# Performance work log

Measured on AMD Instinct MI355X. Metric: run time of the kernel, lower is better.

The kernel has to match this reference:

```python
import jax, jax.numpy as jnp
import numpy as np

H, W = 32, 32
DIM = 768
NUM_BLOCKS = 4
BLOCK = DIM // NUM_BLOCKS
SCALE = 0.02


def setup_inputs() -> dict:
    key = jax.random.key(0)
    k0, k1, k2, k3, k4 = jax.random.split(key, 5)
    B, N, C = 64, H * W, DIM
    x = jax.random.normal(k0, (B, N, C), dtype=jnp.float32)
    w1 = SCALE * jax.random.normal(k1, (2, NUM_BLOCKS, BLOCK, BLOCK), dtype=jnp.float32)
    b1 = SCALE * jax.random.normal(k2, (2, NUM_BLOCKS, BLOCK), dtype=jnp.float32)
    w2 = SCALE * jax.random.normal(k3, (2, NUM_BLOCKS, BLOCK, BLOCK), dtype=jnp.float32)
    b2 = SCALE * jax.random.normal(k4, (2, NUM_BLOCKS, BLOCK), dtype=jnp.float32)
    return {"x": x, "w1": w1, "b1": b1, "w2": w2, "b2": b2}


def _mul(inp, weights):
    # inp: [B, H, Wf, blocks, d], weights: [blocks, d, k]
    return jnp.einsum('...bd,bdk->...bk', inp, weights)


def reference(x, w1, b1, w2, b2):
    B, N, C = x.shape
    xg = x.reshape(B, H, W, C)
    xf = jnp.fft.rfft2(xg, axes=(1, 2), norm='ortho')  # [B, H, W//2+1, C] complex64
    xf = xf.reshape(B, xf.shape[1], xf.shape[2], NUM_BLOCKS, BLOCK)
    xr, xi = xf.real, xf.imag
    # layer 1: complex block-diagonal linear + ReLU
    r1 = jax.nn.relu(_mul(xr, w1[0]) - _mul(xi, w1[1]) + b1[0])
    i1 = jax.nn.relu(_mul(xr, w1[1]) + _mul(xi, w1[0]) + b1[1])
    # layer 2 (faithful to original: imag uses the already-updated real part)
    r2 = _mul(r1, w2[0]) - _mul(i1, w2[1]) + b2[0]
    i2 = _mul(r2, w2[1]) + _mul(i1, w2[0]) + b2[1]
    xc = (r2 + 1j * i2).reshape(B, r2.shape[1], r2.shape[2], C)
    out = jnp.fft.irfft2(xc, s=(H, W), axes=(1, 2), norm='ortho')
    return out.reshape(B, N, C) + jnp.zeros_like(x)  # bias is zeros (self.bias is None)
```

## Files before the change

kernel.cpp:

```cpp
#include <hip/hip_runtime.h>
#include <cstddef>
#include <cstdint>


typedef __attribute__((ext_vector_type(8))) short bf16x8;
typedef __attribute__((ext_vector_type(4))) float f32x4;

namespace {

constexpr int BATCH = 64;
constexpr int WF    = 17;
constexpr int CC    = 768;
constexpr int BLK   = 192;

constexpr size_t W_ELEMS  = 16u * 36864u;
constexpr size_t TW_ELEMS = 8u * 1024u;
constexpr size_t PW_ELEMS = W_ELEMS + TW_ELEMS;

constexpr int PLANE_U = 48 * 512;

constexpr float C32[32] = {
   1.0000000000f,  0.9807852804f,  0.9238795325f,  0.8314696123f,
   0.7071067812f,  0.5555702330f,  0.3826834324f,  0.1950903220f,
   0.0000000000f, -0.1950903220f, -0.3826834324f, -0.5555702330f,
  -0.7071067812f, -0.8314696123f, -0.9238795325f, -0.9807852804f,
  -1.0000000000f, -0.9807852804f, -0.9238795325f, -0.8314696123f,
  -0.7071067812f, -0.5555702330f, -0.3826834324f, -0.1950903220f,
   0.0000000000f,  0.1950903220f,  0.3826834324f,  0.5555702330f,
   0.7071067812f,  0.8314696123f,  0.9238795325f,  0.9807852804f
};
constexpr float S32[32] = {
   0.0000000000f,  0.1950903220f,  0.3826834324f,  0.5555702330f,
   0.7071067812f,  0.8314696123f,  0.9238795325f,  0.9807852804f,
   1.0000000000f,  0.9807852804f,  0.9238795325f,  0.8314696123f,
   0.7071067812f,  0.5555702330f,  0.3826834324f,  0.1950903220f,
   0.0000000000f, -0.1950903220f, -0.3826834324f, -0.5555702330f,
  -0.7071067812f, -0.8314696123f, -0.9238795325f, -0.9807852804f,
  -1.0000000000f, -0.9807852804f, -0.9238795325f, -0.8314696123f,
  -0.7071067812f, -0.5555702330f, -0.3826834324f, -0.1950903220f
};

}

__device__ __forceinline__ ushort f2bf(float f) {
    union { float f; unsigned u; } v; v.f = f;
    const unsigned r = (v.u + 0x7FFFu + ((v.u >> 16) & 1u)) >> 16;
    return (ushort)r;
}
__device__ __forceinline__ uint pk(float lo, float hi) {
    return (uint)f2bf(lo) | ((uint)f2bf(hi) << 16);
}
__device__ __forceinline__ bf16x8 neg8(bf16x8 a) {
    union { bf16x8 v; uint4 u; } t; t.v = a;
    t.u.x ^= 0x80008000u; t.u.y ^= 0x80008000u;
    t.u.z ^= 0x80008000u; t.u.w ^= 0x80008000u;
    return t.v;
}

__global__ __launch_bounds__(256) void k_pack(const float* __restrict__ w1,
                                              const float* __restrict__ w2,
                                              ushort* __restrict__ pw) {
    const unsigned idx = blockIdx.x * 256u + threadIdx.x;
    if (idx < W_ELEMS) {
        const unsigned mi = idx / 36864u;
        const unsigned r  = idx % 36864u;
        const unsigned kk = r / 6144u;
        const unsigned r2 = r % 6144u;
        const unsigned nf = r2 / 512u;
        const unsigned r3 = r2 % 512u;
        const unsigned lane = r3 / 8u;
        const unsigned i  = r3 % 8u;
        const unsigned d   = kk * 32u + (lane >> 4) * 8u + i;
        const unsigned col = nf * 16u + (lane & 15u);
        const unsigned mat = mi >> 2, blk = mi & 3u;
        const float* src;
        if      (mat == 0u) src = w1 + (size_t)(0 * 4 + blk) * BLK * BLK;
        else if (mat == 1u) src = w1 + (size_t)(1 * 4 + blk) * BLK * BLK;
        else if (mat == 2u) src = w2 + (size_t)(0 * 4 + blk) * BLK * BLK;
        else                src = w2 + (size_t)(1 * 4 + blk) * BLK * BLK;
        pw[idx] = f2bf(src[(size_t)d * BLK + col]);
    } else if (idx < PW_ELEMS) {
        const unsigned t = idx - (unsigned)W_ELEMS;
        const unsigned mat = t >> 10;
        const unsigned rr  = t & 1023u;
        const unsigned mf  = rr >> 9;
        const unsigned q   = rr & 511u;
        const unsigned lane = q >> 3, i = q & 7u;
        const unsigned row = mf * 16u + (lane & 15u);
        const unsigned col = (lane >> 4) * 8u + i;
        const unsigned ang = (row * col) & 31u;
        float v;
        if      (mat == 0u) v = C32[ang] * 0.03125f;
        else if (mat == 1u) v = S32[ang] * 0.03125f;
        else if (mat == 2u) v = -S32[ang] * 0.03125f;
        else if (mat == 3u) v = C32[ang];
        else if (mat == 4u) v = S32[ang];
        else if (mat == 5u) v = -S32[ang];
        else if (mat == 6u) {
            if      (col == 0u)  v = 0.03125f;
            else if (col < 16u)  v = 2.f * C32[ang] * 0.03125f;
            else if (col == 16u) v = C32[(16u * row) & 31u] * 0.03125f;
            else                 v = 0.f;
        } else {
            v = (col >= 1u && col <= 15u) ? (-2.f * S32[ang] * 0.03125f) : 0.f;
        }
        pw[idx] = f2bf(v);
    }
}

__global__ __launch_bounds__(256) void k_rfft_w(const float* __restrict__ x,
                                                ushort* __restrict__ spec,
                                                const ushort* __restrict__ pw) {
    __shared__ uint xb[16 * 384];

    const int bid = blockIdx.x;
    const int cq = bid & 3;
    const int hp = (bid >> 2) & 15;
    const int b  = bid >> 6;
    const int tid = threadIdx.x;
    const int wv = tid >> 6, l = tid & 63, lc = l & 15, lg = l >> 4;

#pragma unroll
    for (int it = 0; it < 6; ++it) {
        const int flat = it * 256 + tid;
        const int h  = flat / 768;
        const int rm = flat % 768;
        const int wp = rm / 48;
        const int c4 = rm % 48;
        const float* p = x + ((size_t)(b * 1024 + (hp * 2 + h) * 32 + wp * 2) * CC)
                           + cq * 192 + c4 * 4;
        const float4 a  = *(const float4*)p;
        const float4 bb = *(const float4*)(p + CC);
        uint4 u;
        u.x = pk(a.x, bb.x); u.y = pk(a.y, bb.y);
        u.z = pk(a.z, bb.z); u.w = pk(a.w, bb.w);
        const int col = (h * 192 + c4 * 4) ^ (((wp >> 2) & 3) << 3);
        *(uint4*)&xb[wp * 384 + col] = u;
    }
    __syncthreads();

    const ushort* TW = pw + W_ELEMS;
    bf16x8 ac[2], as[2];
#pragma unroll
    for (int m = 0; m < 2; ++m) {
        ac[m] = *(const bf16x8*)(TW + ((size_t)(3 * 2 + m) * 64 + l) * 8);
        as[m] = *(const bf16x8*)(TW + ((size_t)(5 * 2 + m) * 64 + l) * 8);
    }

    f32x4 aR[2][6] = {}, aI[2][6] = {};
#pragma unroll
    for (int j = 0; j < 6; ++j) {
        const int nf = (j < 3) ? (wv * 3 + j) : (12 + wv * 3 + (j - 3));
        union { bf16x8 v; uint d[4]; } u;
#pragma unroll
        for (int t = 0; t < 4; ++t) {
            const int wp = lg * 4 + t;
            u.d[t] = xb[wp * 384 + ((nf * 16 + lc) ^ (lg << 3))];
        }
#pragma unroll
        for (int m = 0; m < 2; ++m) {
            aR[m][j] = __builtin_amdgcn_mfma_f32_16x16x32_bf16(ac[m], u.v, aR[m][j], 0, 0, 0);
            aI[m][j] = __builtin_amdgcn_mfma_f32_16x16x32_bf16(as[m], u.v, aI[m][j], 0, 0, 0);
        }
    }

    uint* spec32 = (uint*)spec;
    const int swz = (hp & 7) << 1;
#pragma unroll
    for (int m = 0; m < 2; ++m)
#pragma unroll
        for (int j = 0; j < 3; ++j)
#pragma unroll
            for (int r = 0; r < 4; ++r) {
                if (m == 1 && (lg != 0 || r != 0)) continue;
                const int kw = m * 16 + lg * 4 + r;
                const int csub = cq * 12 + wv * 3 + j;
                const size_t pos = ((size_t)(b * WF + kw) * 2) * 12288
                                 + csub * 256 + hp * 16 + (lc ^ swz);
                spec32[pos]         = pk(aR[m][j][r], aR[m][j + 3][r]);
                spec32[pos + 12288] = pk(aI[m][j][r], aI[m][j + 3][r]);
            }
}

__global__ __launch_bounds__(256, 4) void k_fft_mix(
        ushort* __restrict__ spec,
        const ushort* __restrict__ pw,
        const float* __restrict__ b1, const float* __restrict__ b2) {

    __shared__ ushort lds[3][6336];

    const int bid = blockIdx.x;
    const int blk = bid / (BATCH * WF);
    const int rem = bid % (BATCH * WF);
    const int b   = rem / WF;
    const int kw  = rem % WF;
    const int tid = threadIdx.x;
    const int wv = tid >> 6, l = tid & 63, lc = l & 15, lg = l >> 4;

    const size_t gR = ((size_t)(b * WF + kw) * 2) * PLANE_U + blk * 6144;
    const size_t gI = gR + PLANE_U;

#pragma unroll
    for (int j = 0; j < 3; ++j) {
        const int q = tid + 256 * j;
        const int dst = (q >> 6) * 528 + (q & 63) * 8;
        *(uint4*)&lds[0][dst] = *(const uint4*)(spec + gR + q * 8);
        *(uint4*)&lds[1][dst] = *(const uint4*)(spec + gI + q * 8);
    }
    __syncthreads();

    const ushort* TW = pw + W_ELEMS;
    const int col0 = wv * 48;

    {
        bf16x8 xr[3], xi[3];
#pragma unroll
        for (int n = 0; n < 3; ++n) {
            const int csub = wv * 3 + n;
            union { bf16x8 v; uint d[4]; } ur, ui;
#pragma unroll
            for (int t = 0; t < 4; ++t) {
                const int hp = lg * 4 + t;
                const int pos = csub * 528 + hp * 32 + ((lc ^ ((hp & 7) << 1)) << 1);
                ur.d[t] = *(const uint*)&lds[0][pos];
                ui.d[t] = *(const uint*)&lds[1][pos];
            }
            xr[n] = ur.v; xi[n] = ui.v;
        }
        bf16x8 cf[2], sf[2], sfn[2];
#pragma unroll
        for (int m = 0; m < 2; ++m) {
            cf[m]  = *(const bf16x8*)(TW + ((size_t)(0 * 2 + m) * 64 + l) * 8);
            sf[m]  = *(const bf16x8*)(TW + ((size_t)(1 * 2 + m) * 64 + l) * 8);
            sfn[m] = *(const bf16x8*)(TW + ((size_t)(2 * 2 + m) * 64 + l) * 8);
        }
        f32x4 yr[2][3] = {}, yi[2][3] = {};
#pragma unroll
        for (int m = 0; m < 2; ++m)
#pragma unroll
            for (int n = 0; n < 3; ++n) {
                yr[m][n] = __builtin_amdgcn_mfma_f32_16x16x32_bf16(cf[m],  xr[n], yr[m][n], 0, 0, 0);
                yr[m][n] = __builtin_amdgcn_mfma_f32_16x16x32_bf16(sf[m],  xi[n], yr[m][n], 0, 0, 0);
                yi[m][n] = __builtin_amdgcn_mfma_f32_16x16x32_bf16(cf[m],  xi[n], yi[m][n], 0, 0, 0);
                yi[m][n] = __builtin_amdgcn_mfma_f32_16x16x32_bf16(sfn[m], xr[n], yi[m][n], 0, 0, 0);
            }
#pragma unroll
        for (int m = 0; m < 2; ++m)
#pragma unroll
            for (int n = 0; n < 3; ++n)
#pragma unroll
                for (int rp = 0; rp < 2; ++rp) {
                    const uint ur = pk(yr[m][n][2 * rp], yr[m][n][2 * rp + 1]);
                    const uint ui = pk(yi[m][n][2 * rp], yi[m][n][2 * rp + 1]);
                    const int p0 = (wv * 3 + n) * 528 + (m * 16 + lg * 4 + 2 * rp) * 16 + lc;
                    lds[0][p0] = (ushort)ur; lds[0][p0 + 16] = (ushort)(ur >> 16);
                    lds[1][p0] = (ushort)ui; lds[1][p0 + 16] = (ushort)(ui >> 16);
                }
    }
    __syncthreads();

    const ushort* pW1r = pw + (size_t)(0 * 4 + blk) * 36864;
    const ushort* pW1i = pw + (size_t)(1 * 4 + blk) * 36864;
    const ushort* pW2r = pw + (size_t)(2 * 4 + blk) * 36864;
    const ushort* pW2i = pw + (size_t)(3 * 4 + blk) * 36864;

    {
        f32x4 aR[2][3], aI[2][3];
#pragma unroll
        for (int n = 0; n < 3; ++n) {
            const float br = b1[(size_t)(0 * 4 + blk) * BLK + col0 + n * 16 + lc];
            const float bi = b1[(size_t)(1 * 4 + blk) * BLK + col0 + n * 16 + lc];
#pragma unroll
            for (int m = 0; m < 2; ++m) {
                aR[m][n] = (f32x4){br, br, br, br};
                aI[m][n] = (f32x4){bi, bi, bi, bi};
            }
        }
#pragma unroll
        for (int kk = 0; kk < 6; ++kk) {
            const int csubA = 2 * kk + (lg >> 1);
            const int apos  = csubA * 528 + lc * 16 + (lg & 1) * 8;
            bf16x8 ar[2], ai[2], ain[2];
#pragma unroll
            for (int m = 0; m < 2; ++m) {
                ar[m]  = *(const bf16x8*)&lds[0][apos + m * 256];
                ai[m]  = *(const bf16x8*)&lds[1][apos + m * 256];
                ain[m] = neg8(ai[m]);
            }
            bf16x8 wr[3], wi[3];
#pragma unroll
            for (int n = 0; n < 3; ++n) {
                const size_t off = ((size_t)(kk * 12 + wv * 3 + n) * 64 + l) * 8;
                wr[n] = *(const bf16x8*)(pW1r + off);
                wi[n] = *(const bf16x8*)(pW1i + off);
            }
#pragma unroll
            for (int m = 0; m < 2; ++m)
#pragma unroll
                for (int n = 0; n < 3; ++n) {
                    aR[m][n] = __builtin_amdgcn_mfma_f32_16x16x32_bf16(ar[m],  wr[n], aR[m][n], 0, 0, 0);
                    aR[m][n] = __builtin_amdgcn_mfma_f32_16x16x32_bf16(ain[m], wi[n], aR[m][n], 0, 0, 0);
                    aI[m][n] = __builtin_amdgcn_mfma_f32_16x16x32_bf16(ar[m],  wi[n], aI[m][n], 0, 0, 0);
                    aI[m][n] = __builtin_amdgcn_mfma_f32_16x16x32_bf16(ai[m],  wr[n], aI[m][n], 0, 0, 0);
                }
        }
        __syncthreads();
#pragma unroll
        for (int m = 0; m < 2; ++m)
#pragma unroll
            for (int n = 0; n < 3; ++n)
#pragma unroll
                for (int rp = 0; rp < 2; ++rp) {
                    const uint ur = pk(fmaxf(aR[m][n][2 * rp], 0.f), fmaxf(aR[m][n][2 * rp + 1], 0.f));
                    const uint ui = pk(fmaxf(aI[m][n][2 * rp], 0.f), fmaxf(aI[m][n][2 * rp + 1], 0.f));
                    const int p0 = (wv * 3 + n) * 528 + (m * 16 + lg * 4 + 2 * rp) * 16 + lc;
                    lds[0][p0] = (ushort)ur; lds[0][p0 + 16] = (ushort)(ur >> 16);
                    lds[1][p0] = (ushort)ui; lds[1][p0 + 16] = (ushort)(ui >> 16);
                }
    }
    __syncthreads();

    {
        f32x4 cR[2][3];
#pragma unroll
        for (int n = 0; n < 3; ++n) {
            const float br = b2[(size_t)(0 * 4 + blk) * BLK + col0 + n * 16 + lc];
#pragma unroll
            for (int m = 0; m < 2; ++m) cR[m][n] = (f32x4){br, br, br, br};
        }
#pragma unroll
        for (int kk = 0; kk < 6; ++kk) {
            const int csubA = 2 * kk + (lg >> 1);
            const int apos  = csubA * 528 + lc * 16 + (lg & 1) * 8;
            bf16x8 ar[2], ain[2];
#pragma unroll
            for (int m = 0; m < 2; ++m) {
                ar[m]  = *(const bf16x8*)&lds[0][apos + m * 256];
                ain[m] = neg8(*(const bf16x8*)&lds[1][apos + m * 256]);
            }
            bf16x8 wr[3], wi[3];
#pragma unroll
            for (int n = 0; n < 3; ++n) {
                const size_t off = ((size_t)(kk * 12 + wv * 3 + n) * 64 + l) * 8;
                wr[n] = *(const bf16x8*)(pW2r + off);
                wi[n] = *(const bf16x8*)(pW2i + off);
            }
#pragma unroll
            for (int m = 0; m < 2; ++m)
#pragma unroll
                for (int n = 0; n < 3; ++n) {
                    cR[m][n] = __builtin_amdgcn_mfma_f32_16x16x32_bf16(ar[m],  wr[n], cR[m][n], 0, 0, 0);
                    cR[m][n] = __builtin_amdgcn_mfma_f32_16x16x32_bf16(ain[m], wi[n], cR[m][n], 0, 0, 0);
                }
        }
        __syncthreads();
#pragma unroll
        for (int m = 0; m < 2; ++m)
#pragma unroll
            for (int n = 0; n < 3; ++n) {
                const int csub = wv * 3 + n;
#pragma unroll
                for (int rp = 0; rp < 2; ++rp) {
                    const uint p = pk(cR[m][n][2 * rp], cR[m][n][2 * rp + 1]);
                    const int kh0 = m * 16 + lg * 4 + 2 * rp;
                    lds[0][csub * 528 + kh0 * 16 + lc]       = (ushort)p;
                    lds[0][csub * 528 + (kh0 + 1) * 16 + lc] = (ushort)(p >> 16);
                    const int hp = kh0 >> 1;
                    const int post = csub * 528 + hp * 32 + ((lc ^ ((hp & 7) << 1)) << 1);
                    *(uint*)&lds[2][post] = p;
                }
            }
    }
    __syncthreads();

    {
        f32x4 cI[2][3];
#pragma unroll
        for (int n = 0; n < 3; ++n) {
            const float bi = b2[(size_t)(1 * 4 + blk) * BLK + col0 + n * 16 + lc];
#pragma unroll
            for (int m = 0; m < 2; ++m) cI[m][n] = (f32x4){bi, bi, bi, bi};
        }
#pragma unroll
        for (int kk = 0; kk < 6; ++kk) {
            const int csubA = 2 * kk + (lg >> 1);
            const int apos  = csubA * 528 + lc * 16 + (lg & 1) * 8;
            bf16x8 a2[2], i1[2];
#pragma unroll
            for (int m = 0; m < 2; ++m) {
                a2[m] = *(const bf16x8*)&lds[0][apos + m * 256];
                i1[m] = *(const bf16x8*)&lds[1][apos + m * 256];
            }
            bf16x8 wi[3], wr[3];
#pragma unroll
            for (int n = 0; n < 3; ++n) {
                const size_t off = ((size_t)(kk * 12 + wv * 3 + n) * 64 + l) * 8;
                wi[n] = *(const bf16x8*)(pW2i + off);
                wr[n] = *(const bf16x8*)(pW2r + off);
            }
#pragma unroll
            for (int m = 0; m < 2; ++m)
#pragma unroll
                for (int n = 0; n < 3; ++n) {
                    cI[m][n] = __builtin_amdgcn_mfma_f32_16x16x32_bf16(a2[m], wi[n], cI[m][n], 0, 0, 0);
                    cI[m][n] = __builtin_amdgcn_mfma_f32_16x16x32_bf16(i1[m], wr[n], cI[m][n], 0, 0, 0);
                }
        }
        __syncthreads();
#pragma unroll
        for (int m = 0; m < 2; ++m)
#pragma unroll
            for (int n = 0; n < 3; ++n) {
                const int csub = wv * 3 + n;
#pragma unroll
                for (int rp = 0; rp < 2; ++rp) {
                    const int hp = (m * 16 + lg * 4 + 2 * rp) >> 1;
                    const int post = csub * 528 + hp * 32 + ((lc ^ ((hp & 7) << 1)) << 1);
                    *(uint*)&lds[1][post] = pk(cI[m][n][2 * rp], cI[m][n][2 * rp + 1]);
                }
            }
    }

    {
        bf16x8 ci[2], si[2], sn[2];
#pragma unroll
        for (int m = 0; m < 2; ++m) {
            ci[m] = *(const bf16x8*)(TW + ((size_t)(3 * 2 + m) * 64 + l) * 8);
            si[m] = *(const bf16x8*)(TW + ((size_t)(4 * 2 + m) * 64 + l) * 8);
            sn[m] = *(const bf16x8*)(TW + ((size_t)(5 * 2 + m) * 64 + l) * 8);
        }
        bf16x8 r2b[3], i2b[3];
#pragma unroll
        for (int n = 0; n < 3; ++n) {
            const int csub = wv * 3 + n;
            union { bf16x8 v; uint d[4]; } ur, ui;
#pragma unroll
            for (int t = 0; t < 4; ++t) {
                const int hp = lg * 4 + t;
                const int pos = csub * 528 + hp * 32 + ((lc ^ ((hp & 7) << 1)) << 1);
                ur.d[t] = *(const uint*)&lds[2][pos];
                ui.d[t] = *(const uint*)&lds[1][pos];
            }
            r2b[n] = ur.v; i2b[n] = ui.v;
        }
        f32x4 zr[2][3] = {}, zi[2][3] = {};
#pragma unroll
        for (int m = 0; m < 2; ++m)
#pragma unroll
            for (int n = 0; n < 3; ++n) {
                zr[m][n] = __builtin_amdgcn_mfma_f32_16x16x32_bf16(ci[m], r2b[n], zr[m][n], 0, 0, 0);
                zr[m][n] = __builtin_amdgcn_mfma_f32_16x16x32_bf16(sn[m], i2b[n], zr[m][n], 0, 0, 0);
                zi[m][n] = __builtin_amdgcn_mfma_f32_16x16x32_bf16(ci[m], i2b[n], zi[m][n], 0, 0, 0);
                zi[m][n] = __builtin_amdgcn_mfma_f32_16x16x32_bf16(si[m], r2b[n], zi[m][n], 0, 0, 0);
            }
#pragma unroll
        for (int m = 0; m < 2; ++m)
#pragma unroll
            for (int n = 0; n < 3; ++n) {
                const size_t cbase = gR + (size_t)(wv * 3 + n) * 512;
#pragma unroll
                for (int rp = 0; rp < 2; ++rp) {
                    const int hp = (m * 16 + lg * 4 + 2 * rp) >> 1;
                    const size_t pos = cbase + hp * 32 + ((lc ^ ((hp & 7) << 1)) << 1);
                    *(uint*)(spec + pos)           = pk(zr[m][n][2 * rp], zr[m][n][2 * rp + 1]);
                    *(uint*)(spec + pos + PLANE_U) = pk(zi[m][n][2 * rp], zi[m][n][2 * rp + 1]);
                }
            }
    }
}

__global__ __launch_bounds__(256) void k_irfft_w(const ushort* __restrict__ spec,
                                                 float* __restrict__ out,
                                                 const ushort* __restrict__ pw) {
    __shared__ uint rawR[17 * 198];
    __shared__ uint rawI[17 * 198];

    const int bid = blockIdx.x;
    const int cq = bid & 3;
    const int hp = (bid >> 2) & 15;
    const int b  = bid >> 6;
    const int tid = threadIdx.x;
    const int wv = tid >> 6, l = tid & 63, lc = l & 15, lg = l >> 4;

    const uint* spec32 = (const uint*)spec;

#pragma unroll
    for (int it = 0; it < 13; ++it) {
        const int slot = it * 256 + tid;
        if (slot < 3264) {
            const int part = slot & 7;
            const int c2   = slot >> 3;
            const int plane = c2 / 204;
            const int q  = c2 % 204;
            const int kw = q / 12, csub = q % 12;
            const size_t gpos = ((size_t)(b * WF + kw) * 2 + plane) * 12288
                              + (cq * 12 + csub) * 256 + hp * 16 + part * 2;
            const uint2 v = *(const uint2*)(spec32 + gpos);
            uint* dst = plane ? rawI : rawR;
            *(uint2*)&dst[kw * 198 + csub * 16 + part * 2] = v;
        }
    }
    __syncthreads();

    const ushort* TW = pw + W_ELEMS;
    bf16x8 twA[2], twB[2];
#pragma unroll
    for (int m = 0; m < 2; ++m) {
        twA[m] = *(const bf16x8*)(TW + ((size_t)(6 * 2 + m) * 64 + l) * 8);
        twB[m] = *(const bf16x8*)(TW + ((size_t)(7 * 2 + m) * 64 + l) * 8);
    }

    int rowoff[8];
#pragma unroll
    for (int i = 0; i < 8; ++i) {
        int kwv = lg * 8 + i;
        if (kwv > 16) kwv = 16;
        rowoff[i] = kwv * 396;
    }

    const ushort* rr = (const ushort*)rawR;
    const ushort* ri = (const ushort*)rawI;
    const int swz = (hp & 7) << 1;

    f32x4 acc[2][6] = {};
#pragma unroll
    for (int j = 0; j < 6; ++j) {
        const int coll = (wv * 6 + j) * 16 + lc;
        const int h  = coll & 1;
        const int cL = coll >> 1;
        const int bu = ((cL >> 4) * 16 + ((cL & 15) ^ swz)) * 2 + h;
        union { bf16x8 v; ushort s[8]; } fr, fi;
#pragma unroll
        for (int i = 0; i < 8; ++i) {
            fr.s[i] = rr[rowoff[i] + bu];
            fi.s[i] = ri[rowoff[i] + bu];
        }
#pragma unroll
        for (int m = 0; m < 2; ++m) {
            acc[m][j] = __builtin_amdgcn_mfma_f32_16x16x32_bf16(twA[m], fr.v, acc[m][j], 0, 0, 0);
            acc[m][j] = __builtin_amdgcn_mfma_f32_16x16x32_bf16(twB[m], fi.v, acc[m][j], 0, 0, 0);
        }
    }

#pragma unroll
    for (int m = 0; m < 2; ++m)
#pragma unroll
        for (int j = 0; j < 6; ++j) {
            const int coll = (wv * 6 + j) * 16 + lc;
            const int h  = coll & 1;
            const int c  = cq * 192 + (coll >> 1);
#pragma unroll
            for (int r = 0; r < 4; ++r) {
                const int w = m * 16 + lg * 4 + r;
                out[((size_t)(b * 1024 + (hp * 2 + h) * 32 + w)) * CC + c] = acc[m][j][r];
            }
        }
}

extern "C" void kernel_launch(void* const* d_in, const int* in_sizes, int n_in,
                              void* d_out, int out_size, void* d_ws, size_t ws_size,
                              hipStream_t stream) {
    const float* x  = (const float*)d_in[0];
    const float* w1 = (const float*)d_in[1];
    const float* b1 = (const float*)d_in[2];
    const float* w2 = (const float*)d_in[3];
    const float* b2 = (const float*)d_in[4];
    float* out = (float*)d_out;

    ushort* pw   = (ushort*)d_ws;
    ushort* spec = pw + PW_ELEMS;

    k_pack<<<dim3((unsigned)(PW_ELEMS / 256)), dim3(256), 0, stream>>>(w1, w2, pw);
    k_rfft_w<<<dim3(BATCH * 16 * 4), dim3(256), 0, stream>>>(x, spec, pw);
    k_fft_mix<<<dim3(4 * BATCH * WF), dim3(256), 0, stream>>>(spec, pw, b1, b2);
    k_irfft_w<<<dim3(BATCH * 16 * 4), dim3(256), 0, stream>>>(spec, out, pw);
}
```

Baseline: 285.5 us.

## Process two batch items per block in fft_mix to reuse weight fragments

Each k_fft_mix block now handles two batch entries (same kw and channel block), halving the grid and doubling LDS via dynamic shared memory. Weight fragments loaded from global memory per kk step are reused across both items, halving weight traffic per unit of work. In exchange, accumulator register use doubles and occupancy bounds drop from 4 to 2 blocks per CU, so fewer waves are available to hide latency.

```diff
diff --git a/kernel.cpp b/kernel.cpp
--- a/kernel.cpp
+++ b/kernel.cpp
@@ -182,30 +182,36 @@
             }
 }
 
-__global__ __launch_bounds__(256, 4) void k_fft_mix(
+__global__ __launch_bounds__(256, 2) void k_fft_mix(
         ushort* __restrict__ spec,
         const ushort* __restrict__ pw,
         const float* __restrict__ b1, const float* __restrict__ b2) {
 
-    __shared__ ushort lds[3][6336];
+    extern __shared__ ushort ldsraw[];
+    typedef ushort Regions[3][6336];
+    Regions* lds = (Regions*)ldsraw;
 
     const int bid = blockIdx.x;
-    const int blk = bid / (BATCH * WF);
-    const int rem = bid % (BATCH * WF);
-    const int b   = rem / WF;
+    const int blk = bid / (32 * WF);
+    const int rem = bid % (32 * WF);
+    const int bp  = rem / WF;
     const int kw  = rem % WF;
     const int tid = threadIdx.x;
     const int wv = tid >> 6, l = tid & 63, lc = l & 15, lg = l >> 4;
 
-    const size_t gR = ((size_t)(b * WF + kw) * 2) * PLANE_U + blk * 6144;
-    const size_t gI = gR + PLANE_U;
+    size_t gRt[2];
+    gRt[0] = ((size_t)((bp * 2) * WF + kw) * 2) * PLANE_U + blk * 6144;
+    gRt[1] = gRt[0] + (size_t)WF * 2 * PLANE_U;
 
 #pragma unroll
     for (int j = 0; j < 3; ++j) {
         const int q = tid + 256 * j;
         const int dst = (q >> 6) * 528 + (q & 63) * 8;
-        *(uint4*)&lds[0][dst] = *(const uint4*)(spec + gR + q * 8);
-        *(uint4*)&lds[1][dst] = *(const uint4*)(spec + gI + q * 8);
+#pragma unroll
+        for (int t = 0; t < 2; ++t) {
+            *(uint4*)&lds[t][0][dst] = *(const uint4*)(spec + gRt[t] + q * 8);
+            *(uint4*)&lds[t][1][dst] = *(const uint4*)(spec + gRt[t] + PLANE_U + q * 8);
+        }
     }
     __syncthreads();
 
@@ -213,20 +219,6 @@
     const int col0 = wv * 48;
 
     {
-        bf16x8 xr[3], xi[3];
-#pragma unroll
-        for (int n = 0; n < 3; ++n) {
-            const int csub = wv * 3 + n;
-            union { bf16x8 v; uint d[4]; } ur, ui;
-#pragma unroll
-            for (int t = 0; t < 4; ++t) {
-                const int hp = lg * 4 + t;
-                const int pos = csub * 528 + hp * 32 + ((lc ^ ((hp & 7) << 1)) << 1);
-                ur.d[t] = *(const uint*)&lds[0][pos];
-                ui.d[t] = *(const uint*)&lds[1][pos];
-            }
-            xr[n] = ur.v; xi[n] = ui.v;
-        }
         bf16x8 cf[2], sf[2], sfn[2];
 #pragma unroll
         for (int m = 0; m < 2; ++m) {
@@ -234,28 +226,45 @@
             sf[m]  = *(const bf16x8*)(TW + ((size_t)(1 * 2 + m) * 64 + l) * 8);
             sfn[m] = *(const bf16x8*)(TW + ((size_t)(2 * 2 + m) * 64 + l) * 8);
         }
-        f32x4 yr[2][3] = {}, yi[2][3] = {};
-#pragma unroll
-        for (int m = 0; m < 2; ++m)
+#pragma unroll
+        for (int t = 0; t < 2; ++t) {
+            bf16x8 xr[3], xi[3];
 #pragma unroll
             for (int n = 0; n < 3; ++n) {
-                yr[m][n] = __builtin_amdgcn_mfma_f32_16x16x32_bf16(cf[m],  xr[n], yr[m][n], 0, 0, 0);
-                yr[m][n] = __builtin_amdgcn_mfma_f32_16x16x32_bf16(sf[m],  xi[n], yr[m][n], 0, 0, 0);
-                yi[m][n] = __builtin_amdgcn_mfma_f32_16x16x32_bf16(cf[m],  xi[n], yi[m][n], 0, 0, 0);
-                yi[m][n] = __builtin_amdgcn_mfma_f32_16x16x32_bf16(sfn[m], xr[n], yi[m][n], 0, 0, 0);
-            }
-#pragma unroll
-        for (int m = 0; m < 2; ++m)
-#pragma unroll
-            for (int n = 0; n < 3; ++n)
-#pragma unroll
-                for (int rp = 0; rp < 2; ++rp) {
-                    const uint ur = pk(yr[m][n][2 * rp], yr[m][n][2 * rp + 1]);
-                    const uint ui = pk(yi[m][n][2 * rp], yi[m][n][2 * rp + 1]);
-                    const int p0 = (wv * 3 + n) * 528 + (m * 16 + lg * 4 + 2 * rp) * 16 + lc;
-                    lds[0][p0] = (ushort)ur; lds[0][p0 + 16] = (ushort)(ur >> 16);
-                    lds[1][p0] = (ushort)ui; lds[1][p0 + 16] = (ushort)(ui >> 16);
-                }
+                const int csub = wv * 3 + n;
+                union { bf16x8 v; uint d[4]; } ur, ui;
+#pragma unroll
+                for (int tt = 0; tt < 4; ++tt) {
+                    const int hp = lg * 4 + tt;
+                    const int pos = csub * 528 + hp * 32 + ((lc ^ ((hp & 7) << 1)) << 1);
+                    ur.d[tt] = *(const uint*)&lds[t][0][pos];
+                    ui.d[tt] = *(const uint*)&lds[t][1][pos];
+                }
+                xr[n] = ur.v; xi[n] = ui.v;
+            }
+            f32x4 yr[2][3] = {}, yi[2][3] = {};
+#pragma unroll
+            for (int m = 0; m < 2; ++m)
+#pragma unroll
+                for (int n = 0; n < 3; ++n) {
+                    yr[m][n] = __builtin_amdgcn_mfma_f32_16x16x32_bf16(cf[m],  xr[n], yr[m][n], 0, 0, 0);
+                    yr[m][n] = __builtin_amdgcn_mfma_f32_16x16x32_bf16(sf[m],  xi[n], yr[m][n], 0, 0, 0);
+                    yi[m][n] = __builtin_amdgcn_mfma_f32_16x16x32_bf16(cf[m],  xi[n], yi[m][n], 0, 0, 0);
+                    yi[m][n] = __builtin_amdgcn_mfma_f32_16x16x32_bf16(sfn[m], xr[n], yi[m][n], 0, 0, 0);
+                }
+#pragma unroll
+            for (int m = 0; m < 2; ++m)
+#pragma unroll
+                for (int n = 0; n < 3; ++n)
+#pragma unroll
+                    for (int rp = 0; rp < 2; ++rp) {
+                        const uint ur = pk(yr[m][n][2 * rp], yr[m][n][2 * rp + 1]);
+                        const uint ui = pk(yi[m][n][2 * rp], yi[m][n][2 * rp + 1]);
+                        const int p0 = (wv * 3 + n) * 528 + (m * 16 + lg * 4 + 2 * rp) * 16 + lc;
+                        lds[t][0][p0] = (ushort)ur; lds[t][0][p0 + 16] = (ushort)(ur >> 16);
+                        lds[t][1][p0] = (ushort)ui; lds[t][1][p0 + 16] = (ushort)(ui >> 16);
+                    }
+        }
     }
     __syncthreads();
 
@@ -265,28 +274,23 @@
     const ushort* pW2i = pw + (size_t)(3 * 4 + blk) * 36864;
 
     {
-        f32x4 aR[2][3], aI[2][3];
+        f32x4 aR[2][2][3], aI[2][2][3];
 #pragma unroll
         for (int n = 0; n < 3; ++n) {
             const float br = b1[(size_t)(0 * 4 + blk) * BLK + col0 + n * 16 + lc];
             const float bi = b1[(size_t)(1 * 4 + blk) * BLK + col0 + n * 16 + lc];
 #pragma unroll
-            for (int m = 0; m < 2; ++m) {
-                aR[m][n] = (f32x4){br, br, br, br};
-                aI[m][n] = (f32x4){bi, bi, bi, bi};
-            }
+            for (int t = 0; t < 2; ++t)
+#pragma unroll
+                for (int m = 0; m < 2; ++m) {
+                    aR[t][m][n] = (f32x4){br, br, br, br};
+                    aI[t][m][n] = (f32x4){bi, bi, bi, bi};
+                }
         }
 #pragma unroll
         for (int kk = 0; kk < 6; ++kk) {
             const int csubA = 2 * kk + (lg >> 1);
             const int apos  = csubA * 528 + lc * 16 + (lg & 1) * 8;
-            bf16x8 ar[2], ai[2], ain[2];
-#pragma unroll
-            for (int m = 0; m < 2; ++m) {
-                ar[m]  = *(const bf16x8*)&lds[0][apos + m * 256];
-                ai[m]  = *(const bf16x8*)&lds[1][apos + m * 256];
-                ain[m] = neg8(ai[m]);
-            }
             bf16x8 wr[3], wi[3];
 #pragma unroll
             for (int n = 0; n < 3; ++n) {
@@ -295,49 +299,57 @@
                 wi[n] = *(const bf16x8*)(pW1i + off);
             }
 #pragma unroll
+            for (int t = 0; t < 2; ++t) {
+                bf16x8 ar[2], ai[2], ain[2];
+#pragma unroll
+                for (int m = 0; m < 2; ++m) {
+                    ar[m]  = *(const bf16x8*)&lds[t][0][apos + m * 256];
+                    ai[m]  = *(const bf16x8*)&lds[t][1][apos + m * 256];
+                    ain[m] = neg8(ai[m]);
+                }
+#pragma unroll
+                for (int m = 0; m < 2; ++m)
+#pragma unroll
+                    for (int n = 0; n < 3; ++n) {
+                        aR[t][m][n] = __builtin_amdgcn_mfma_f32_16x16x32_bf16(ar[m],  wr[n], aR[t][m][n], 0, 0, 0);
+                        aR[t][m][n] = __builtin_amdgcn_mfma_f32_16x16x32_bf16(ain[m], wi[n], aR[t][m][n], 0, 0, 0);
+                        aI[t][m][n] = __builtin_amdgcn_mfma_f32_16x16x32_bf16(ar[m],  wi[n], aI[t][m][n], 0, 0, 0);
+                        aI[t][m][n] = __builtin_amdgcn_mfma_f32_16x16x32_bf16(ai[m],  wr[n], aI[t][m][n], 0, 0, 0);
+                    }
+            }
+        }
+        __syncthreads();
+#pragma unroll
+        for (int t = 0; t < 2; ++t)
+#pragma unroll
             for (int m = 0; m < 2; ++m)
 #pragma unroll
-                for (int n = 0; n < 3; ++n) {
-                    aR[m][n] = __builtin_amdgcn_mfma_f32_16x16x32_bf16(ar[m],  wr[n], aR[m][n], 0, 0, 0);
-                    aR[m][n] = __builtin_amdgcn_mfma_f32_16x16x32_bf16(ain[m], wi[n], aR[m][n], 0, 0, 0);
-                    aI[m][n] = __builtin_amdgcn_mfma_f32_16x16x32_bf16(ar[m],  wi[n], aI[m][n], 0, 0, 0);
-                    aI[m][n] = __builtin_amdgcn_mfma_f32_16x16x32_bf16(ai[m],  wr[n], aI[m][n], 0, 0, 0);
-                }
-        }
-        __syncthreads();
-#pragma unroll
-        for (int m = 0; m < 2; ++m)
-#pragma unroll
-            for (int n = 0; n < 3; ++n)
-#pragma unroll
-                for (int rp = 0; rp < 2; ++rp) {
-                    const uint ur = pk(fmaxf(aR[m][n][2 * rp], 0.f), fmaxf(aR[m][n][2 * rp + 1], 0.f));
-                    const uint ui = pk(fmaxf(aI[m][n][2 * rp], 0.f), fmaxf(aI[m][n][2 * rp + 1], 0.f));
-                    const int p0 = (wv * 3 + n) * 528 + (m * 16 + lg * 4 + 2 * rp) * 16 + lc;
-                    lds[0][p0] = (ushort)ur; lds[0][p0 + 16] = (ushort)(ur >> 16);
-                    lds[1][p0] = (ushort)ui; lds[1][p0 + 16] = (ushort)(ui >> 16);
-                }
+                for (int n = 0; n < 3; ++n)
+#pragma unroll
+                    for (int rp = 0; rp < 2; ++rp) {
+                        const uint ur = pk(fmaxf(aR[t][m][n][2 * rp], 0.f), fmaxf(aR[t][m][n][2 * rp + 1], 0.f));
+                        const uint ui = pk(fmaxf(aI[t][m][n][2 * rp], 0.f), fmaxf(aI[t][m][n][2 * rp + 1], 0.f));
+                        const int p0 = (wv * 3 + n) * 528 + (m * 16 + lg * 4 + 2 * rp) * 16 + lc;
+                        lds[t][0][p0] = (ushort)ur; lds[t][0][p0 + 16] = (ushort)(ur >> 16);
+                        lds[t][1][p0] = (ushort)ui; lds[t][1][p0 + 16] = (ushort)(ui >> 16);
+                    }
     }
     __syncthreads();
 
     {
-        f32x4 cR[2][3];
+        f32x4 cR[2][2][3];
 #pragma unroll
         for (int n = 0; n < 3; ++n) {
             const float br = b2[(size_t)(0 * 4 + blk) * BLK + col0 + n * 16 + lc];
 #pragma unroll
-            for (int m = 0; m < 2; ++m) cR[m][n] = (f32x4){br, br, br, br};
+            for (int t = 0; t < 2; ++t)
+#pragma unroll
+                for (int m = 0; m < 2; ++m) cR[t][m][n] = (f32x4){br, br, br, br};
         }
 #pragma unroll
         for (int kk = 0; kk < 6; ++kk) {
             const int csubA = 2 * kk + (lg >> 1);
             const int apos  = csubA * 528 + lc * 16 + (lg & 1) * 8;
-            bf16x8 ar[2], ain[2];
-#pragma unroll
-            for (int m = 0; m < 2; ++m) {
-                ar[m]  = *(const bf16x8*)&lds[0][apos + m * 256];
-                ain[m] = neg8(*(const bf16x8*)&lds[1][apos + m * 256]);
-            }
             bf16x8 wr[3], wi[3];
 #pragma unroll
             for (int n = 0; n < 3; ++n) {
@@ -346,51 +358,58 @@
                 wi[n] = *(const bf16x8*)(pW2i + off);
             }
 #pragma unroll
+            for (int t = 0; t < 2; ++t) {
+                bf16x8 ar[2], ain[2];
+#pragma unroll
+                for (int m = 0; m < 2; ++m) {
+                    ar[m]  = *(const bf16x8*)&lds[t][0][apos + m * 256];
+                    ain[m] = neg8(*(const bf16x8*)&lds[t][1][apos + m * 256]);
+                }
+#pragma unroll
+                for (int m = 0; m < 2; ++m)
+#pragma unroll
+                    for (int n = 0; n < 3; ++n) {
+                        cR[t][m][n] = __builtin_amdgcn_mfma_f32_16x16x32_bf16(ar[m],  wr[n], cR[t][m][n], 0, 0, 0);
+                        cR[t][m][n] = __builtin_amdgcn_mfma_f32_16x16x32_bf16(ain[m], wi[n], cR[t][m][n], 0, 0, 0);
+                    }
+            }
+        }
+        __syncthreads();
+#pragma unroll
+        for (int t = 0; t < 2; ++t)
+#pragma unroll
             for (int m = 0; m < 2; ++m)
 #pragma unroll
                 for (int n = 0; n < 3; ++n) {
-                    cR[m][n] = __builtin_amdgcn_mfma_f32_16x16x32_bf16(ar[m],  wr[n], cR[m][n], 0, 0, 0);
-                    cR[m][n] = __builtin_amdgcn_mfma_f32_16x16x32_bf16(ain[m], wi[n], cR[m][n], 0, 0, 0);
-                }
-        }
-        __syncthreads();
-#pragma unroll
-        for (int m = 0; m < 2; ++m)
-#pragma unroll
-            for (int n = 0; n < 3; ++n) {
-                const int csub = wv * 3 + n;
-#pragma unroll
-                for (int rp = 0; rp < 2; ++rp) {
-                    const uint p = pk(cR[m][n][2 * rp], cR[m][n][2 * rp + 1]);
-                    const int kh0 = m * 16 + lg * 4 + 2 * rp;
-                    lds[0][csub * 528 + kh0 * 16 + lc]       = (ushort)p;
-                    lds[0][csub * 528 + (kh0 + 1) * 16 + lc] = (ushort)(p >> 16);
-                    const int hp = kh0 >> 1;
-                    const int post = csub * 528 + hp * 32 + ((lc ^ ((hp & 7) << 1)) << 1);
-                    *(uint*)&lds[2][post] = p;
-                }
-            }
+                    const int csub = wv * 3 + n;
+#pragma unroll
+                    for (int rp = 0; rp < 2; ++rp) {
+                        const uint p = pk(cR[t][m][n][2 * rp], cR[t][m][n][2 * rp + 1]);
+                        const int kh0 = m * 16 + lg * 4 + 2 * rp;
+                        lds[t][0][csub * 528 + kh0 * 16 + lc]       = (ushort)p;
+                        lds[t][0][csub * 528 + (kh0 + 1) * 16 + lc] = (ushort)(p >> 16);
+                        const int hp = kh0 >> 1;
+                        const int post = csub * 528 + hp * 32 + ((lc ^ ((hp & 7) << 1)) << 1);
+                        *(uint*)&lds[t][2][post] = p;
+                    }
+                }
     }
     __syncthreads();
 
     {
-        f32x4 cI[2][3];
+        f32x4 cI[2][2][3];
 #pragma unroll
         for (int n = 0; n < 3; ++n) {
             const float bi = b2[(size_t)(1 * 4 + blk) * BLK + col0 + n * 16 + lc];
 #pragma unroll
-            for (int m = 0; m < 2; ++m) cI[m][n] = (f32x4){bi, bi, bi, bi};
+            for (int t = 0; t < 2; ++t)
+#pragma unroll
+                for (int m = 0; m < 2; ++m) cI[t][m][n] = (f32x4){bi, bi, bi, bi};
         }
 #pragma unroll
         for (int kk = 0; kk < 6; ++kk) {
             const int csubA = 2 * kk + (lg >> 1);
             const int apos  = csubA * 528 + lc * 16 + (lg & 1) * 8;
-            bf16x8 a2[2], i1[2];
-#pragma unroll
-            for (int m = 0; m < 2; ++m) {
-                a2[m] = *(const bf16x8*)&lds[0][apos + m * 256];
-                i1[m] = *(const bf16x8*)&lds[1][apos + m * 256];
-            }
             bf16x8 wi[3], wr[3];
 #pragma unroll
             for (int n = 0; n < 3; ++n) {
@@ -399,26 +418,37 @@
                 wr[n] = *(const bf16x8*)(pW2r + off);
             }
 #pragma unroll
+            for (int t = 0; t < 2; ++t) {
+                bf16x8 a2[2], i1[2];
+#pragma unroll
+                for (int m = 0; m < 2; ++m) {
+                    a2[m] = *(const bf16x8*)&lds[t][0][apos + m * 256];
+                    i1[m] = *(const bf16x8*)&lds[t][1][apos + m * 256];
+                }
+#pragma unroll
+                for (int m = 0; m < 2; ++m)
+#pragma unroll
+                    for (int n = 0; n < 3; ++n) {
+                        cI[t][m][n] = __builtin_amdgcn_mfma_f32_16x16x32_bf16(a2[m], wi[n], cI[t][m][n], 0, 0, 0);
+                        cI[t][m][n] = __builtin_amdgcn_mfma_f32_16x16x32_bf16(i1[m], wr[n], cI[t][m][n], 0, 0, 0);
+                    }
+            }
+        }
+        __syncthreads();
+#pragma unroll
+        for (int t = 0; t < 2; ++t)
+#pragma unroll
             for (int m = 0; m < 2; ++m)
 #pragma unroll
                 for (int n = 0; n < 3; ++n) {
-                    cI[m][n] = __builtin_amdgcn_mfma_f32_16x16x32_bf16(a2[m], wi[n], cI[m][n], 0, 0, 0);
-                    cI[m][n] = __builtin_amdgcn_mfma_f32_16x16x32_bf16(i1[m], wr[n], cI[m][n], 0, 0, 0);
-                }
-        }
-        __syncthreads();
-#pragma unroll
-        for (int m = 0; m < 2; ++m)
-#pragma unroll
-            for (int n = 0; n < 3; ++n) {
-                const int csub = wv * 3 + n;
-#pragma unroll
-                for (int rp = 0; rp < 2; ++rp) {
-                    const int hp = (m * 16 + lg * 4 + 2 * rp) >> 1;
-                    const int post = csub * 528 + hp * 32 + ((lc ^ ((hp & 7) << 1)) << 1);
-                    *(uint*)&lds[1][post] = pk(cI[m][n][2 * rp], cI[m][n][2 * rp + 1]);
-                }
-            }
+                    const int csub = wv * 3 + n;
+#pragma unroll
+                    for (int rp = 0; rp < 2; ++rp) {
+                        const int hp = (m * 16 + lg * 4 + 2 * rp) >> 1;
+                        const int post = csub * 528 + hp * 32 + ((lc ^ ((hp & 7) << 1)) << 1);
+                        *(uint*)&lds[t][1][post] = pk(cI[t][m][n][2 * rp], cI[t][m][n][2 * rp + 1]);
+                    }
+                }
     }
 
     {
@@ -429,43 +459,46 @@
             si[m] = *(const bf16x8*)(TW + ((size_t)(4 * 2 + m) * 64 + l) * 8);
             sn[m] = *(const bf16x8*)(TW + ((size_t)(5 * 2 + m) * 64 + l) * 8);
         }
-        bf16x8 r2b[3], i2b[3];
-#pragma unroll
-        for (int n = 0; n < 3; ++n) {
-            const int csub = wv * 3 + n;
-            union { bf16x8 v; uint d[4]; } ur, ui;
-#pragma unroll
-            for (int t = 0; t < 4; ++t) {
-                const int hp = lg * 4 + t;
-                const int pos = csub * 528 + hp * 32 + ((lc ^ ((hp & 7) << 1)) << 1);
-                ur.d[t] = *(const uint*)&lds[2][pos];
-                ui.d[t] = *(const uint*)&lds[1][pos];
-            }
-            r2b[n] = ur.v; i2b[n] = ui.v;
-        }
-        f32x4 zr[2][3] = {}, zi[2][3] = {};
-#pragma unroll
-        for (int m = 0; m < 2; ++m)
+#pragma unroll
+        for (int t = 0; t < 2; ++t) {
+            bf16x8 r2b[3], i2b[3];
 #pragma unroll
             for (int n = 0; n < 3; ++n) {
-                zr[m][n] = __builtin_amdgcn_mfma_f32_16x16x32_bf16(ci[m], r2b[n], zr[m][n], 0, 0, 0);
-                zr[m][n] = __builtin_amdgcn_mfma_f32_16x16x32_bf16(sn[m], i2b[n], zr[m][n], 0, 0, 0);
-                zi[m][n] = __builtin_amdgcn_mfma_f32_16x16x32_bf16(ci[m], i2b[n], zi[m][n], 0, 0, 0);
-                zi[m][n] = __builtin_amdgcn_mfma_f32_16x16x32_bf16(si[m], r2b[n], zi[m][n], 0, 0, 0);
-            }
-#pragma unroll
-        for (int m = 0; m < 2; ++m)
-#pragma unroll
-            for (int n = 0; n < 3; ++n) {
-                const size_t cbase = gR + (size_t)(wv * 3 + n) * 512;
-#pragma unroll
-                for (int rp = 0; rp < 2; ++rp) {
-                    const int hp = (m * 16 + lg * 4 + 2 * rp) >> 1;
-                    const size_t pos = cbase + hp * 32 + ((lc ^ ((hp & 7) << 1)) << 1);
-                    *(uint*)(spec + pos)           = pk(zr[m][n][2 * rp], zr[m][n][2 * rp + 1]);
-                    *(uint*)(spec + pos + PLANE_U) = pk(zi[m][n][2 * rp], zi[m][n][2 * rp + 1]);
-                }
-            }
+                const int csub = wv * 3 + n;
+                union { bf16x8 v; uint d[4]; } ur, ui;
+#pragma unroll
+                for (int tt = 0; tt < 4; ++tt) {
+                    const int hp = lg * 4 + tt;
+                    const int pos = csub * 528 + hp * 32 + ((lc ^ ((hp & 7) << 1)) << 1);
+                    ur.d[tt] = *(const uint*)&lds[t][2][pos];
+                    ui.d[tt] = *(const uint*)&lds[t][1][pos];
+                }
+                r2b[n] = ur.v; i2b[n] = ui.v;
+            }
+            f32x4 zr[2][3] = {}, zi[2][3] = {};
+#pragma unroll
+            for (int m = 0; m < 2; ++m)
+#pragma unroll
+                for (int n = 0; n < 3; ++n) {
+                    zr[m][n] = __builtin_amdgcn_mfma_f32_16x16x32_bf16(ci[m], r2b[n], zr[m][n], 0, 0, 0);
+                    zr[m][n] = __builtin_amdgcn_mfma_f32_16x16x32_bf16(sn[m], i2b[n], zr[m][n], 0, 0, 0);
+                    zi[m][n] = __builtin_amdgcn_mfma_f32_16x16x32_bf16(ci[m], i2b[n], zi[m][n], 0, 0, 0);
+                    zi[m][n] = __builtin_amdgcn_mfma_f32_16x16x32_bf16(si[m], r2b[n], zi[m][n], 0, 0, 0);
+                }
+#pragma unroll
+            for (int m = 0; m < 2; ++m)
+#pragma unroll
+                for (int n = 0; n < 3; ++n) {
+                    const size_t cbase = gRt[t] + (size_t)(wv * 3 + n) * 512;
+#pragma unroll
+                    for (int rp = 0; rp < 2; ++rp) {
+                        const int hp = (m * 16 + lg * 4 + 2 * rp) >> 1;
+                        const size_t pos = cbase + hp * 32 + ((lc ^ ((hp & 7) << 1)) << 1);
+                        *(uint*)(spec + pos)           = pk(zr[m][n][2 * rp], zr[m][n][2 * rp + 1]);
+                        *(uint*)(spec + pos + PLANE_U) = pk(zi[m][n][2 * rp], zi[m][n][2 * rp + 1]);
+                    }
+                }
+        }
     }
 }
 
@@ -570,8 +603,14 @@
     ushort* pw   = (ushort*)d_ws;
     ushort* spec = pw + PW_ELEMS;
 
+    constexpr unsigned K2_LDS = 2u * 3u * 6336u * 2u;
+
+    (void)hipFuncSetAttribute((const void*)k_fft_mix,
+                              hipFuncAttributeMaxDynamicSharedMemorySize,
+                              (int)K2_LDS);
+
     k_pack<<<dim3((unsigned)(PW_ELEMS / 256)), dim3(256), 0, stream>>>(w1, w2, pw);
     k_rfft_w<<<dim3(BATCH * 16 * 4), dim3(256), 0, stream>>>(x, spec, pw);
-    k_fft_mix<<<dim3(4 * BATCH * WF), dim3(256), 0, stream>>>(spec, pw, b1, b2);
+    k_fft_mix<<<dim3(4 * 32 * WF), dim3(256), K2_LDS, stream>>>(spec, pw, b1, b2);
     k_irfft_w<<<dim3(BATCH * 16 * 4), dim3(256), 0, stream>>>(spec, out, pw);
 }
```

Measured after the change: 258.5 us. -9.5%, faster.

## Precompute composed W2 matrices so layer-2 imag part skips dependency on r2

Applied to the files above, without the earlier changes.

The dependent second-layer imaginary output i2 = r2·W2i + i1·W2r is expanded algebraically using r2 = r1·W2r − i1·W2i + b2r. The expanded weights (W2r·W2i, W2r − W2i·W2i) and the folded bias are precomputed in the pack kernel. Both real and imaginary outputs can then be computed from r1/i1 without a sync and LDS round trip, and one LDS buffer is dropped. The trade-offs are an expensive per-element O(192) dot product inside the pack kernel (run every call), changed bf16 rounding of the composed weights, and removal of the occupancy launch bound.

```diff
diff --git a/kernel.cpp b/kernel.cpp
--- a/kernel.cpp
+++ b/kernel.cpp
@@ -13,9 +13,10 @@
 constexpr int CC    = 768;
 constexpr int BLK   = 192;
 
-constexpr size_t W_ELEMS  = 16u * 36864u;
+constexpr size_t W_ELEMS  = 24u * 36864u;
 constexpr size_t TW_ELEMS = 8u * 1024u;
-constexpr size_t PW_ELEMS = W_ELEMS + TW_ELEMS;
+constexpr size_t B2P_USH  = 768u * 2u;
+constexpr size_t PW_ELEMS = W_ELEMS + TW_ELEMS + B2P_USH;
 
 constexpr int PLANE_U = 48 * 512;
 
@@ -59,6 +60,7 @@
 
 __global__ __launch_bounds__(256) void k_pack(const float* __restrict__ w1,
                                               const float* __restrict__ w2,
+                                              const float* __restrict__ b2,
                                               ushort* __restrict__ pw) {
     const unsigned idx = blockIdx.x * 256u + threadIdx.x;
     if (idx < W_ELEMS) {
@@ -70,16 +72,29 @@
         const unsigned r3 = r2 % 512u;
         const unsigned lane = r3 / 8u;
         const unsigned i  = r3 % 8u;
-        const unsigned d   = kk * 32u + (lane >> 4) * 8u + i;
-        const unsigned col = nf * 16u + (lane & 15u);
+        const int d   = (int)(kk * 32u + (lane >> 4) * 8u + i);
+        const int col = (int)(nf * 16u + (lane & 15u));
         const unsigned mat = mi >> 2, blk = mi & 3u;
-        const float* src;
-        if      (mat == 0u) src = w1 + (size_t)(0 * 4 + blk) * BLK * BLK;
-        else if (mat == 1u) src = w1 + (size_t)(1 * 4 + blk) * BLK * BLK;
-        else if (mat == 2u) src = w2 + (size_t)(0 * 4 + blk) * BLK * BLK;
-        else                src = w2 + (size_t)(1 * 4 + blk) * BLK * BLK;
-        pw[idx] = f2bf(src[(size_t)d * BLK + col]);
-    } else if (idx < PW_ELEMS) {
+        float v;
+        if      (mat == 0u) v = w1[(size_t)(0 * 4 + blk) * 36864 + d * BLK + col];
+        else if (mat == 1u) v = w1[(size_t)(1 * 4 + blk) * 36864 + d * BLK + col];
+        else if (mat == 2u) v = w2[(size_t)(0 * 4 + blk) * 36864 + d * BLK + col];
+        else if (mat == 3u) v = w2[(size_t)(1 * 4 + blk) * 36864 + d * BLK + col];
+        else if (mat == 4u) {
+            const float* R = w2 + (size_t)(0 * 4 + blk) * 36864;
+            const float* I = w2 + (size_t)(1 * 4 + blk) * 36864;
+            float s = 0.f;
+            for (int e = 0; e < BLK; ++e) s = fmaf(R[d * BLK + e], I[e * BLK + col], s);
+            v = s;
+        } else {
+            const float* R = w2 + (size_t)(0 * 4 + blk) * 36864;
+            const float* I = w2 + (size_t)(1 * 4 + blk) * 36864;
+            float s = 0.f;
+            for (int e = 0; e < BLK; ++e) s = fmaf(I[d * BLK + e], I[e * BLK + col], s);
+            v = R[d * BLK + col] - s;
+        }
+        pw[idx] = f2bf(v);
+    } else if (idx < W_ELEMS + TW_ELEMS) {
         const unsigned t = idx - (unsigned)W_ELEMS;
         const unsigned mat = t >> 10;
         const unsigned rr  = t & 1023u;
@@ -105,6 +120,14 @@
             v = (col >= 1u && col <= 15u) ? (-2.f * S32[ang] * 0.03125f) : 0.f;
         }
         pw[idx] = f2bf(v);
+    } else if (idx < W_ELEMS + TW_ELEMS + 768u) {
+        const unsigned t = idx - (unsigned)(W_ELEMS + TW_ELEMS);
+        const unsigned blk = t / 192u, k = t % 192u;
+        const float* I  = w2 + (size_t)(1 * 4 + blk) * 36864;
+        const float* br = b2 + (size_t)(0 * 4 + blk) * BLK;
+        float s = b2[(size_t)(1 * 4 + blk) * BLK + k];
+        for (int d = 0; d < BLK; ++d) s = fmaf(br[d], I[d * BLK + k], s);
+        ((float*)(pw + W_ELEMS + TW_ELEMS))[t] = s;
     }
 }
 
@@ -182,12 +205,12 @@
             }
 }
 
-__global__ __launch_bounds__(256, 4) void k_fft_mix(
+__global__ __launch_bounds__(256) void k_fft_mix(
         ushort* __restrict__ spec,
         const ushort* __restrict__ pw,
         const float* __restrict__ b1, const float* __restrict__ b2) {
 
-    __shared__ ushort lds[3][6336];
+    __shared__ ushort lds[2][6336];
 
     const int bid = blockIdx.x;
     const int blk = bid / (BATCH * WF);
@@ -263,6 +286,8 @@
     const ushort* pW1i = pw + (size_t)(1 * 4 + blk) * 36864;
     const ushort* pW2r = pw + (size_t)(2 * 4 + blk) * 36864;
     const ushort* pW2i = pw + (size_t)(3 * 4 + blk) * 36864;
+    const ushort* pWa  = pw + (size_t)(4 * 4 + blk) * 36864;
+    const ushort* pWb  = pw + (size_t)(5 * 4 + blk) * 36864;
 
     {
         f32x4 aR[2][3], aI[2][3];
@@ -321,7 +346,7 @@
     __syncthreads();
 
     {
-        f32x4 cR[2][3];
+        f32x4 cR[2][3], cI[2][3];
 #pragma unroll
         for (int n = 0; n < 3; ++n) {
             const float br = b2[(size_t)(0 * 4 + blk) * BLK + col0 + n * 16 + lc];
@@ -353,31 +378,10 @@
                     cR[m][n] = __builtin_amdgcn_mfma_f32_16x16x32_bf16(ain[m], wi[n], cR[m][n], 0, 0, 0);
                 }
         }
-        __syncthreads();
-#pragma unroll
-        for (int m = 0; m < 2; ++m)
-#pragma unroll
-            for (int n = 0; n < 3; ++n) {
-                const int csub = wv * 3 + n;
-#pragma unroll
-                for (int rp = 0; rp < 2; ++rp) {
-                    const uint p = pk(cR[m][n][2 * rp], cR[m][n][2 * rp + 1]);
-                    const int kh0 = m * 16 + lg * 4 + 2 * rp;
-                    lds[0][csub * 528 + kh0 * 16 + lc]       = (ushort)p;
-                    lds[0][csub * 528 + (kh0 + 1) * 16 + lc] = (ushort)(p >> 16);
-                    const int hp = kh0 >> 1;
-                    const int post = csub * 528 + hp * 32 + ((lc ^ ((hp & 7) << 1)) << 1);
-                    *(uint*)&lds[2][post] = p;
-                }
-            }
-    }
-    __syncthreads();
-
-    {
-        f32x4 cI[2][3];
+        const float* b2p = (const float*)(pw + W_ELEMS + TW_ELEMS);
 #pragma unroll
         for (int n = 0; n < 3; ++n) {
-            const float bi = b2[(size_t)(1 * 4 + blk) * BLK + col0 + n * 16 + lc];
+            const float bi = b2p[blk * BLK + col0 + n * 16 + lc];
 #pragma unroll
             for (int m = 0; m < 2; ++m) cI[m][n] = (f32x4){bi, bi, bi, bi};
         }
@@ -385,25 +389,25 @@
         for (int kk = 0; kk < 6; ++kk) {
             const int csubA = 2 * kk + (lg >> 1);
             const int apos  = csubA * 528 + lc * 16 + (lg & 1) * 8;
-            bf16x8 a2[2], i1[2];
+            bf16x8 ar[2], ai[2];
 #pragma unroll
             for (int m = 0; m < 2; ++m) {
-                a2[m] = *(const bf16x8*)&lds[0][apos + m * 256];
-                i1[m] = *(const bf16x8*)&lds[1][apos + m * 256];
-            }
-            bf16x8 wi[3], wr[3];
+                ar[m] = *(const bf16x8*)&lds[0][apos + m * 256];
+                ai[m] = *(const bf16x8*)&lds[1][apos + m * 256];
+            }
+            bf16x8 wa[3], wb[3];
 #pragma unroll
             for (int n = 0; n < 3; ++n) {
                 const size_t off = ((size_t)(kk * 12 + wv * 3 + n) * 64 + l) * 8;
-                wi[n] = *(const bf16x8*)(pW2i + off);
-                wr[n] = *(const bf16x8*)(pW2r + off);
+                wa[n] = *(const bf16x8*)(pWa + off);
+                wb[n] = *(const bf16x8*)(pWb + off);
             }
 #pragma unroll
             for (int m = 0; m < 2; ++m)
 #pragma unroll
                 for (int n = 0; n < 3; ++n) {
-                    cI[m][n] = __builtin_amdgcn_mfma_f32_16x16x32_bf16(a2[m], wi[n], cI[m][n], 0, 0, 0);
-                    cI[m][n] = __builtin_amdgcn_mfma_f32_16x16x32_bf16(i1[m], wr[n], cI[m][n], 0, 0, 0);
+                    cI[m][n] = __builtin_amdgcn_mfma_f32_16x16x32_bf16(ar[m], wa[n], cI[m][n], 0, 0, 0);
+                    cI[m][n] = __builtin_amdgcn_mfma_f32_16x16x32_bf16(ai[m], wb[n], cI[m][n], 0, 0, 0);
                 }
         }
         __syncthreads();
@@ -416,6 +420,7 @@
                 for (int rp = 0; rp < 2; ++rp) {
                     const int hp = (m * 16 + lg * 4 + 2 * rp) >> 1;
                     const int post = csub * 528 + hp * 32 + ((lc ^ ((hp & 7) << 1)) << 1);
+                    *(uint*)&lds[0][post] = pk(cR[m][n][2 * rp], cR[m][n][2 * rp + 1]);
                     *(uint*)&lds[1][post] = pk(cI[m][n][2 * rp], cI[m][n][2 * rp + 1]);
                 }
             }
@@ -438,7 +443,7 @@
             for (int t = 0; t < 4; ++t) {
                 const int hp = lg * 4 + t;
                 const int pos = csub * 528 + hp * 32 + ((lc ^ ((hp & 7) << 1)) << 1);
-                ur.d[t] = *(const uint*)&lds[2][pos];
+                ur.d[t] = *(const uint*)&lds[0][pos];
                 ui.d[t] = *(const uint*)&lds[1][pos];
             }
             r2b[n] = ur.v; i2b[n] = ui.v;
@@ -570,7 +575,8 @@
     ushort* pw   = (ushort*)d_ws;
     ushort* spec = pw + PW_ELEMS;
 
-    k_pack<<<dim3((unsigned)(PW_ELEMS / 256)), dim3(256), 0, stream>>>(w1, w2, pw);
+    const unsigned packThreads = (unsigned)(W_ELEMS + TW_ELEMS + 768u);
+    k_pack<<<dim3((packThreads + 255u) / 256u), dim3(256), 0, stream>>>(w1, w2, b2, pw);
     k_rfft_w<<<dim3(BATCH * 16 * 4), dim3(256), 0, stream>>>(x, spec, pw);
     k_fft_mix<<<dim3(4 * BATCH * WF), dim3(256), 0, stream>>>(spec, pw, b1, b2);
     k_irfft_w<<<dim3(BATCH * 16 * 4), dim3(256), 0, stream>>>(spec, out, pw);
```

After: 337.2 us. +18.1%, slower.
